# Optimization experiments

Measured on AMD Instinct MI355X. Metric: run time of the kernel, lower is better.

## Reference

```python
import jax, jax.numpy as jnp
import numpy as np

N = 100000
E = 1600000
DIN = 128
H = 4
C1 = 32   # hidden_dim per head, layer 1
C2 = 64   # output_dim, layer 2 (heads=1)
NEG_SLOPE = 0.2


def setup_inputs() -> dict:
    key = jax.random.key(0)
    ks = jax.random.split(key, 16)
    x = jax.random.normal(ks[0], (N, DIN), dtype=jnp.float32)
    src = jax.random.randint(ks[1], (E,), 0, N, dtype=jnp.int64)
    off = jax.random.randint(ks[2], (E,), 1, N, dtype=jnp.int64)
    dst = (src + off) % N  # guaranteed no self loops
    edge_index = jnp.stack([src, dst], axis=0)
    edge_weight = jax.random.uniform(ks[3], (E,), dtype=jnp.float32)
    g = 0.1
    # layer 1 params (heads=4, concat)
    W1 = jax.random.normal(ks[4], (DIN, H * C1), dtype=jnp.float32) * g
    att_src1 = jax.random.normal(ks[5], (H, C1), dtype=jnp.float32) * g
    att_dst1 = jax.random.normal(ks[6], (H, C1), dtype=jnp.float32) * g
    att_edge1 = jax.random.normal(ks[7], (H, C1), dtype=jnp.float32) * g
    We1 = jax.random.normal(ks[8], (1, H * C1), dtype=jnp.float32) * g
    b1 = jnp.zeros((H * C1,), dtype=jnp.float32)
    # layer 2 params (heads=1, no concat)
    W2 = jax.random.normal(ks[9], (H * C1, C2), dtype=jnp.float32) * g
    att_src2 = jax.random.normal(ks[10], (1, C2), dtype=jnp.float32) * g
    att_dst2 = jax.random.normal(ks[11], (1, C2), dtype=jnp.float32) * g
    att_edge2 = jax.random.normal(ks[12], (1, C2), dtype=jnp.float32) * g
    We2 = jax.random.normal(ks[13], (1, C2), dtype=jnp.float32) * g
    b2 = jnp.zeros((C2,), dtype=jnp.float32)
    return dict(x=x, edge_index=edge_index, edge_weight=edge_weight,
                W1=W1, att_src1=att_src1, att_dst1=att_dst1, att_edge1=att_edge1, We1=We1, b1=b1,
                W2=W2, att_src2=att_src2, att_dst2=att_dst2, att_edge2=att_edge2, We2=We2, b2=b2)


def gat_conv(x, src, dst, ew, W, a_src, a_dst, a_edge, We, b, heads, out_ch, concat):
    n = x.shape[0]
    xs = (x @ W).reshape(n, heads, out_ch)                 # [N,H,C]
    alpha_src = (xs * a_src[None]).sum(-1)                 # [N,H]
    alpha_dst = (xs * a_dst[None]).sum(-1)                 # [N,H]
    e = (ew[:, None] @ We).reshape(-1, heads, out_ch)      # [E,H,C]
    alpha_edge = (e * a_edge[None]).sum(-1)                # [E,H]
    alpha = alpha_src[src] + alpha_dst[dst] + alpha_edge   # [E,H]
    alpha = jax.nn.leaky_relu(alpha, NEG_SLOPE)
    # segment softmax over destination nodes (every node has a self loop)
    m = jax.ops.segment_max(alpha, dst, num_segments=n)
    ex = jnp.exp(alpha - m[dst])
    s = jax.ops.segment_sum(ex, dst, num_segments=n)
    att = ex / (s[dst] + 1e-16)                            # [E,H]
    out = jax.ops.segment_sum(xs[src] * att[:, :, None], dst, num_segments=n)  # [N,H,C]
    out = out.reshape(n, heads * out_ch) if concat else out.mean(axis=1)
    return out + b


def reference(x, edge_index, edge_weight,
              W1, att_src1, att_dst1, att_edge1, We1, b1,
              W2, att_src2, att_dst2, att_edge2, We2, b2):
    n = x.shape[0]
    src, dst = edge_index[0], edge_index[1]
    # add self loops with fill_value='mean' for edge weights (PyG default)
    si = jnp.arange(n, dtype=src.dtype)
    src2 = jnp.concatenate([src, si])
    dst2 = jnp.concatenate([dst, si])
    ew2 = jnp.concatenate([edge_weight, jnp.full((n,), edge_weight.mean(), dtype=edge_weight.dtype)])
    h = gat_conv(x, src2, dst2, ew2, W1, att_src1, att_dst1, att_edge1, We1, b1, H, C1, True)
    h = jax.nn.elu(h)
    # dropout is identity in eval mode
    out = gat_conv(h, src2, dst2, ew2, W2, att_src2, att_dst2, att_edge2, We2, b2, 1, C2, False)
    return out
```

## Files before the change

### kernel.cpp

```cpp
#include <hip/hip_runtime.h>
#include <math.h>

#define NN 100000
#define NE 1600000
#define DIN 128
#define NH 4
#define C1 32
#define C2 64
#define NEG 0.2f

#define SCAN_CHUNK 1024
#define NBLK ((NN + SCAN_CHUNK - 1) / SCAN_CHUNK)

#define NBUCK 8
#define BUCKN (NN / NBUCK)
#define CAPB 300000
#define BIN_CHUNK 4096
#define NBINBLK ((NE + BIN_CHUNK - 1) / BIN_CHUNK)

typedef __attribute__((ext_vector_type(8))) short bf16x8;
typedef __attribute__((ext_vector_type(4))) float f32x4;

__device__ __forceinline__ unsigned bf16rtn(float f) {
    unsigned b = __float_as_uint(f);
    return (b + 0x7FFFu + ((b >> 16) & 1u)) >> 16;
}
__device__ __forceinline__ unsigned pack2bf(float lo, float hi) {
    return bf16rtn(lo) | (bf16rtn(hi) << 16);
}

__global__ void k_setup(const float* __restrict__ We1, const float* __restrict__ ae1,
                        const float* __restrict__ We2, const float* __restrict__ ae2,
                        float* __restrict__ params) {
    __shared__ float sm[128];
    int t = threadIdx.x;
    sm[t] = We1[t] * ae1[t];
    __syncthreads();
    if (t < 4) {
        float s = 0.f;
        for (int c = 0; c < 32; c++) s += sm[t * 32 + c];
        params[2 + t] = s;
    }
    __syncthreads();
    if (t < 64) sm[t] = We2[t] * ae2[t];
    __syncthreads();
    if (t == 0) {
        float s = 0.f;
        for (int c = 0; c < 64; c++) s += sm[c];
        params[6] = s;
        params[1] = params[0] / (float)NE;
    }
}

__global__ void k_wprep(const float* __restrict__ W1, const float* __restrict__ W2,
                        uint4* __restrict__ wfrag1, uint4* __restrict__ wfrag2) {
    int t = blockIdx.x * 256 + threadIdx.x;
    if (t < 2048) {
        int f = t >> 6, l = t & 63;
        int n = f & 7, kc = f >> 3;
        int col = n * 16 + (l & 15);
        int kb = kc * 32 + (l >> 4) * 8;
        const float* p = W1 + (size_t)kb * 128 + col;
        uint4 pk;
        pk.x = pack2bf(p[0], p[128]);
        pk.y = pack2bf(p[256], p[384]);
        pk.z = pack2bf(p[512], p[640]);
        pk.w = pack2bf(p[768], p[896]);
        wfrag1[t] = pk;
    } else if (t < 3072) {
        int s = t - 2048;
        int f = s >> 6, l = s & 63;
        int n = f & 3, kc = f >> 2;
        int col = n * 16 + (l & 15);
        int kb = kc * 32 + (l >> 4) * 8;
        const float* p = W2 + (size_t)kb * 64 + col;
        uint4 pk;
        pk.x = pack2bf(p[0], p[64]);
        pk.y = pack2bf(p[128], p[192]);
        pk.z = pack2bf(p[256], p[320]);
        pk.w = pack2bf(p[384], p[448]);
        wfrag2[s] = pk;
    }
}

__global__ void k_binA(const int* __restrict__ srcI, const int* __restrict__ dstI,
                       const float* __restrict__ ew, int* __restrict__ bcur,
                       int* __restrict__ bdst, int2* __restrict__ bse,
                       float* __restrict__ params) {
    __shared__ int hcnt[NBUCK], hbase[NBUCK], hoff[NBUCK];
    int t = threadIdx.x;
    int e0 = blockIdx.x * BIN_CHUNK;
    if (t < NBUCK) hcnt[t] = 0;
    __syncthreads();
    for (int i = t; i < BIN_CHUNK; i += 256) {
        int e = e0 + i;
        if (e < NE) atomicAdd(&hcnt[dstI[e] / BUCKN], 1);
    }
    __syncthreads();
    if (t < NBUCK) { hbase[t] = atomicAdd(&bcur[t], hcnt[t]); hoff[t] = 0; }
    __syncthreads();
    float locw = 0.f;
    for (int i = t; i < BIN_CHUNK; i += 256) {
        int e = e0 + i;
        if (e < NE) {
            int d = dstI[e];
            float w = ew[e];
            locw += w;
            int b = d / BUCKN;
            int p = b * CAPB + hbase[b] + atomicAdd(&hoff[b], 1);
            bdst[p] = d;
            bse[p] = make_int2(srcI[e], __float_as_int(w));
        }
    }
    for (int o = 32; o > 0; o >>= 1) locw += __shfl_down(locw, o, 64);
    if ((t & 63) == 0) atomicAdd(&params[0], locw);
}

__global__ void k_histB(const int* __restrict__ bdst, const int* __restrict__ bcur,
                        int* __restrict__ deg) {
    int b = blockIdx.x & (NBUCK - 1);
    int slice = blockIdx.x >> 3;
    int cnt = bcur[b];
    int lo = b * CAPB;
    int per = (cnt + 255) / 256;
    int s0 = lo + slice * per;
    int s1 = min(s0 + per, lo + cnt);
    for (int i = s0 + threadIdx.x; i < s1; i += 256)
        atomicAdd(&deg[bdst[i]], 1);
}

__global__ void k_scanA(const int* __restrict__ deg, int* __restrict__ bsum) {
    __shared__ int ws[4];
    int b = blockIdx.x;
    int base = b * SCAN_CHUNK;
    int t = threadIdx.x;
    int s = 0;
    for (int i = t; i < SCAN_CHUNK; i += 256) {
        int idx = base + i;
        if (idx < NN) s += deg[idx];
    }
    for (int o = 32; o > 0; o >>= 1) s += __shfl_down(s, o, 64);
    int lane = t & 63, wid = t >> 6;
    if (lane == 0) ws[wid] = s;
    __syncthreads();
    if (t == 0) bsum[b] = ws[0] + ws[1] + ws[2] + ws[3];
}

__global__ void k_scanB(const int* __restrict__ bsum, int* __restrict__ bpre,
                        int* __restrict__ rowptr) {
    __shared__ int wtot[2];
    int t = threadIdx.x;
    int lane = t & 63, wid = t >> 6;
    int v = (t < NBLK) ? bsum[t] : 0;
    int inc = v;
    for (int o = 1; o < 64; o <<= 1) { int u = __shfl_up(inc, o, 64); if (lane >= o) inc += u; }
    if (lane == 63) wtot[wid] = inc;
    __syncthreads();
    if (wid == 1) inc += wtot[0];
    if (t < NBLK) bpre[t] = inc - v;
    if (t == NBLK - 1) rowptr[NN] = inc;
}

__global__ void k_scanC(const int* __restrict__ deg, const int* __restrict__ bpre,
                        int* __restrict__ rowptr, int* __restrict__ cursor) {
    __shared__ int wtot[4];
    int b = blockIdx.x;
    int t = threadIdx.x;
    int lane = t & 63, wid = t >> 6;
    int idx0 = b * SCAN_CHUNK + t * 4;
    int d[4];
    int s = 0;
    #pragma unroll
    for (int j = 0; j < 4; j++) {
        int idx = idx0 + j;
        d[j] = (idx < NN) ? deg[idx] : 0;
        s += d[j];
    }
    int inc = s;
    for (int o = 1; o < 64; o <<= 1) { int u = __shfl_up(inc, o, 64); if (lane >= o) inc += u; }
    if (lane == 63) wtot[wid] = inc;
    __syncthreads();
    int add = bpre[b];
    for (int w = 0; w < wid; w++) add += wtot[w];
    int excl = inc - s + add;
    #pragma unroll
    for (int j = 0; j < 4; j++) {
        int idx = idx0 + j;
        if (idx < NN) { rowptr[idx] = excl; cursor[idx] = excl; }
        excl += d[j];
    }
}

__global__ void k_binB(const int* __restrict__ bdst, const int2* __restrict__ bse,
                       const int* __restrict__ bcur, int* __restrict__ cursor,
                       int2* __restrict__ edge2) {
    int b = blockIdx.x & (NBUCK - 1);
    int slice = blockIdx.x >> 3;
    int cnt = bcur[b];
    int lo = b * CAPB;
    int per = (cnt + 255) / 256;
    int s0 = lo + slice * per;
    int s1 = min(s0 + per, lo + cnt);
    for (int i = s0 + threadIdx.x; i < s1; i += 256) {
        int d = bdst[i];
        int idx = atomicAdd(&cursor[d], 1);
        edge2[idx] = bse[i];
    }
}


__global__ void __launch_bounds__(256, 4)
k_gemm1(const float* __restrict__ x, const uint4* __restrict__ wfrag1,
        const float* __restrict__ asv, const float* __restrict__ adv,
        unsigned* __restrict__ xs1b, float* __restrict__ as1, float* __restrict__ ad1) {
    __shared__ uint4 smem[2112];
    int t = threadIdx.x;
    for (int i = t; i < 2048; i += 256) smem[i] = wfrag1[i];
    __syncthreads();
    int wid = t >> 6, lane = t & 63;
    int r0 = blockIdx.x * 64 + wid * 16;
    int rowA = r0 + (lane & 15);
    int kb = (lane >> 4) * 8;
    bf16x8 afr[4];
    if (rowA < NN) {
        const float* xr = x + (size_t)rowA * 128 + kb;
        #pragma unroll
        for (int kc = 0; kc < 4; kc++) {
            float4 u0 = *(const float4*)(xr + kc * 32);
            float4 u1 = *(const float4*)(xr + kc * 32 + 4);
            uint4 p = make_uint4(pack2bf(u0.x, u0.y), pack2bf(u0.z, u0.w),
                                 pack2bf(u1.x, u1.y), pack2bf(u1.z, u1.w));
            afr[kc] = *(bf16x8*)&p;
        }
    } else {
        uint4 z = make_uint4(0u, 0u, 0u, 0u);
        #pragma unroll
        for (int kc = 0; kc < 4; kc++) afr[kc] = *(bf16x8*)&z;
    }
    f32x4 acc[8];
    #pragma unroll
    for (int n = 0; n < 8; n++) acc[n] = (f32x4){0.f, 0.f, 0.f, 0.f};
    #pragma unroll
    for (int kc = 0; kc < 4; kc++) {
        #pragma unroll
        for (int n = 0; n < 8; n++) {
            uint4 bw = smem[(kc * 8 + n) * 64 + lane];
            acc[n] = __builtin_amdgcn_mfma_f32_16x16x32_bf16(afr[kc], *(bf16x8*)&bw, acc[n], 0, 0, 0);
        }
    }
    __syncthreads();
    float* ef = (float*)smem + wid * 2112;
    #pragma unroll
    for (int n = 0; n < 8; n++) {
        #pragma unroll
        for (int r = 0; r < 4; r++) {
            int rw = (lane >> 4) * 4 + r;
            int col = n * 16 + (lane & 15);
            ef[rw * 132 + (col >> 5) * 33 + (col & 31)] = acc[n][r];
        }
    }
    __syncthreads();
    int rw = lane >> 2, head = lane & 3;
    int row = r0 + rw;
    if (row < NN) {
        const float* rb = ef + rw * 132 + head * 33;
        const float* av = asv + head * 32;
        const float* dv = adv + head * 32;
        unsigned* orow = xs1b + (size_t)row * 64 + head * 16;
        float ps = 0.f, pd = 0.f;
        #pragma unroll
        for (int j = 0; j < 4; j++) {
            float v[8];
            #pragma unroll
            for (int e = 0; e < 8; e++) {
                v[e] = rb[8 * j + e];
                ps += v[e] * av[8 * j + e];
                pd += v[e] * dv[8 * j + e];
            }
            uint4 pk = make_uint4(pack2bf(v[0], v[1]), pack2bf(v[2], v[3]),
                                  pack2bf(v[4], v[5]), pack2bf(v[6], v[7]));
            *(uint4*)(orow + 4 * j) = pk;
        }
        as1[row * 4 + head] = ps;
        ad1[row * 4 + head] = pd;
    }
}


__global__ void k_agg1(const unsigned* __restrict__ xs1b, const float* __restrict__ as1,
                       const float* __restrict__ ad1, const int* __restrict__ rowptr,
                       const int2* __restrict__ edge2,
                       const float* __restrict__ params, const float* __restrict__ b1,
                       unsigned* __restrict__ h1b) {
    int wid = threadIdx.x >> 6, lane = threadIdx.x & 63;
    int n = blockIdx.x * 4 + wid;
    if (n >= NN) return;
    int h4 = lane & 3;
    int h  = lane >> 4;
    float ceP  = params[2 + h4];
    float adnP = ad1[n * 4 + h4];
    float meanw = params[1];
    float aself = as1[n * 4 + h] + ad1[n * 4 + h] + meanw * params[2 + h];
    aself = aself > 0.f ? aself : NEG * aself;
    float qs = __expf(aself);
    unsigned us = xs1b[(size_t)n * 64 + lane];
    float s  = qs;
    float ax = qs * __uint_as_float(us << 16);
    float ay = qs * __uint_as_float(us & 0xFFFF0000u);
    int lo = rowptr[n], hi = rowptr[n + 1];
    for (int base = lo; base < hi; base += 16) {
        int e = lane >> 2;
        int idx = base + e;
        int cx = 0;
        float q = 0.f;
        if (idx < hi) {
            int2 cv = edge2[idx];
            cx = cv.x;
            float a = as1[cx * 4 + h4] + adnP + __int_as_float(cv.y) * ceP;
            a = a > 0.f ? a : NEG * a;
            q = __expf(a);
        }
        int m = hi - base; if (m > 16) m = 16;
        int j = 0;
        for (; j + 8 <= m; j += 8) {
            int cj[8]; float qj[8]; unsigned vv[8];
            #pragma unroll
            for (int u = 0; u < 8; u++) {
                cj[u] = __shfl(cx, 4 * (j + u), 64);
                qj[u] = __shfl(q, 4 * (j + u) + h, 64);
            }
            #pragma unroll
            for (int u = 0; u < 8; u++) vv[u] = xs1b[(size_t)cj[u] * 64 + lane];
            #pragma unroll
            for (int u = 0; u < 8; u++) {
                s += qj[u];
                ax += qj[u] * __uint_as_float(vv[u] << 16);
                ay += qj[u] * __uint_as_float(vv[u] & 0xFFFF0000u);
            }
        }
        for (; j < m; j++) {
            int cj = __shfl(cx, 4 * j, 64);
            float qj = __shfl(q, 4 * j + h, 64);
            unsigned u = xs1b[(size_t)cj * 64 + lane];
            s += qj;
            ax += qj * __uint_as_float(u << 16);
            ay += qj * __uint_as_float(u & 0xFFFF0000u);
        }
    }
    float inv = 1.0f / (s + 1e-16f);
    float o0 = ax * inv + b1[2 * lane];
    float o1 = ay * inv + b1[2 * lane + 1];
    o0 = o0 > 0.f ? o0 : (__expf(o0) - 1.0f);
    o1 = o1 > 0.f ? o1 : (__expf(o1) - 1.0f);
    h1b[(size_t)n * 64 + lane] = pack2bf(o0, o1);
}


__global__ void __launch_bounds__(256, 6)
k_gemm2(const unsigned* __restrict__ h1b, const uint4* __restrict__ wfrag2,
        const float* __restrict__ asv, const float* __restrict__ adv,
        unsigned* __restrict__ xs2b, float* __restrict__ as2, float* __restrict__ ad2) {
    __shared__ uint4 smem[1056];
    int t = threadIdx.x;
    for (int i = t; i < 1024; i += 256) smem[i] = wfrag2[i];
    __syncthreads();
    int wid = t >> 6, lane = t & 63;
    int r0 = blockIdx.x * 64 + wid * 16;
    int rowA = r0 + (lane & 15);
    bf16x8 afr[4];
    if (rowA < NN) {
        const uint4* hr = (const uint4*)(h1b + (size_t)rowA * 64);
        #pragma unroll
        for (int kc = 0; kc < 4; kc++) {
            uint4 p = hr[kc * 4 + (lane >> 4)];
            afr[kc] = *(bf16x8*)&p;
        }
    } else {
        uint4 z = make_uint4(0u, 0u, 0u, 0u);
        #pragma unroll
        for (int kc = 0; kc < 4; kc++) afr[kc] = *(bf16x8*)&z;
    }
    f32x4 acc[4];
    #pragma unroll
    for (int n = 0; n < 4; n++) acc[n] = (f32x4){0.f, 0.f, 0.f, 0.f};
    #pragma unroll
    for (int kc = 0; kc < 4; kc++) {
        #pragma unroll
        for (int n = 0; n < 4; n++) {
            uint4 bw = smem[(kc * 4 + n) * 64 + lane];
            acc[n] = __builtin_amdgcn_mfma_f32_16x16x32_bf16(afr[kc], *(bf16x8*)&bw, acc[n], 0, 0, 0);
        }
    }
    __syncthreads();
    float* ef = (float*)smem + wid * 1056;
    #pragma unroll
    for (int n = 0; n < 4; n++) {
        #pragma unroll
        for (int r = 0; r < 4; r++) {
            int rw = (lane >> 4) * 4 + r;
            int col = n * 16 + (lane & 15);
            ef[rw * 66 + (col >> 5) * 33 + (col & 31)] = acc[n][r];
        }
    }
    __syncthreads();
    int rw = lane >> 2, q = lane & 3;
    int row = r0 + rw;
    const float* rb = ef + rw * 66 + (q >> 1) * 33 + (q & 1) * 16;
    const float* av = asv + q * 16;
    const float* dv = adv + q * 16;
    float ps = 0.f, pd = 0.f;
    unsigned pk[4];
    #pragma unroll
    for (int j = 0; j < 2; j++) {
        float v[8];
        #pragma unroll
        for (int e = 0; e < 8; e++) {
            v[e] = rb[8 * j + e];
            ps += v[e] * av[8 * j + e];
            pd += v[e] * dv[8 * j + e];
        }
        pk[0] = pack2bf(v[0], v[1]); pk[1] = pack2bf(v[2], v[3]);
        pk[2] = pack2bf(v[4], v[5]); pk[3] = pack2bf(v[6], v[7]);
        if (row < NN)
            *(uint4*)(xs2b + (size_t)row * 32 + q * 8 + 4 * j) = make_uint4(pk[0], pk[1], pk[2], pk[3]);
    }
    ps += __shfl_xor(ps, 1, 64); ps += __shfl_xor(ps, 2, 64);
    pd += __shfl_xor(pd, 1, 64); pd += __shfl_xor(pd, 2, 64);
    if (q == 0 && row < NN) { as2[row] = ps; ad2[row] = pd; }
}


__global__ void k_agg2(const unsigned short* __restrict__ xs2h, const float* __restrict__ as2,
                       const float* __restrict__ ad2, const int* __restrict__ rowptr,
                       const int2* __restrict__ edge2,
                       const float* __restrict__ params, const float* __restrict__ b2,
                       float* __restrict__ out) {
    int wid = threadIdx.x >> 6, lane = threadIdx.x & 63;
    int n = blockIdx.x * 4 + wid;
    if (n >= NN) return;
    float ce = params[6];
    float meanw = params[1];
    float adn = ad2[n];
    float aself = as2[n] + adn + meanw * ce;
    aself = aself > 0.f ? aself : NEG * aself;
    float qs = __expf(aself);
    float s = qs;
    float ac = qs * __uint_as_float(((unsigned)xs2h[(size_t)n * 64 + lane]) << 16);
    int lo = rowptr[n], hi = rowptr[n + 1];
    for (int base = lo; base < hi; base += 64) {
        int idx = base + lane;
        int cx = 0;
        float q = 0.f;
        if (idx < hi) {
            int2 cv = edge2[idx];
            cx = cv.x;
            float a = as2[cx] + adn + __int_as_float(cv.y) * ce;
            a = a > 0.f ? a : NEG * a;
            q = __expf(a);
        }
        int m = hi - base; if (m > 64) m = 64;
        int j = 0;
        for (; j + 8 <= m; j += 8) {
            int cj[8]; float qj[8]; unsigned short vv[8];
            #pragma unroll
            for (int u = 0; u < 8; u++) {
                cj[u] = __shfl(cx, j + u, 64);
                qj[u] = __shfl(q, j + u, 64);
            }
            #pragma unroll
            for (int u = 0; u < 8; u++) vv[u] = xs2h[(size_t)cj[u] * 64 + lane];
            #pragma unroll
            for (int u = 0; u < 8; u++) {
                s += qj[u];
                ac += qj[u] * __uint_as_float(((unsigned)vv[u]) << 16);
            }
        }
        for (; j < m; j++) {
            int cj = __shfl(cx, j, 64);
            float qj = __shfl(q, j, 64);
            float v = __uint_as_float(((unsigned)xs2h[(size_t)cj * 64 + lane]) << 16);
            s += qj;
            ac += qj * v;
        }
    }
    out[(size_t)n * 64 + lane] = ac / (s + 1e-16f) + b2[lane];
}

extern "C" void kernel_launch(void* const* d_in, const int* in_sizes, int n_in,
                              void* d_out, int out_size, void* d_ws, size_t ws_size,
                              hipStream_t stream) {
    const float* x    = (const float*)d_in[0];
    const int*   ei   = (const int*)d_in[1];
    const float* ew   = (const float*)d_in[2];
    const float* W1   = (const float*)d_in[3];
    const float* as1v = (const float*)d_in[4];
    const float* ad1v = (const float*)d_in[5];
    const float* ae1v = (const float*)d_in[6];
    const float* We1  = (const float*)d_in[7];
    const float* b1   = (const float*)d_in[8];
    const float* W2   = (const float*)d_in[9];
    const float* as2v = (const float*)d_in[10];
    const float* ad2v = (const float*)d_in[11];
    const float* ae2v = (const float*)d_in[12];
    const float* We2  = (const float*)d_in[13];
    const float* b2   = (const float*)d_in[14];
    const int* srcI = ei;
    const int* dstI = ei + NE;

    float* wsf = (float*)d_ws;
    size_t off = 0;
    auto alloc = [&](size_t nelts) { float* p = wsf + off; off += (nelts + 63) & ~(size_t)63; return p; };
    float*    params = alloc(64);
    int*      deg    = (int*)alloc(NN);
    int*      bcur   = (int*)alloc(64);
    int*      rowptr = (int*)alloc(NN + 1);
    int*      cursor = (int*)alloc(NN);
    int*      bsum   = (int*)alloc(NBLK);
    int*      bpre   = (int*)alloc(NBLK);
    uint4*    wfrag1 = (uint4*)alloc(8192);
    uint4*    wfrag2 = (uint4*)alloc(4096);
    size_t    binsOff = off;
    int*      bdst   = (int*)alloc((size_t)NBUCK * CAPB);
    int2*     bse    = (int2*)alloc((size_t)NBUCK * CAPB * 2);
    int2*     edge2  = (int2*)alloc((size_t)NE * 2);
    float*    as1    = alloc(NN * 4);
    float*    ad1    = alloc(NN * 4);
    unsigned* h1b    = (unsigned*)alloc((size_t)NN * 64);
    unsigned* xs1b   = (unsigned*)(wsf + binsOff);
    unsigned* xs2b   = xs1b;
    float*    as2 = as1;
    float*    ad2 = ad1;

    hipMemsetAsync(d_ws, 0, (64 + 100032 + 64) * sizeof(float), stream);

    k_wprep<<<12, 256, 0, stream>>>(W1, W2, wfrag1, wfrag2);
    k_binA <<<NBINBLK, 256, 0, stream>>>(srcI, dstI, ew, bcur, bdst, bse, params);
    k_histB<<<2048, 256, 0, stream>>>(bdst, bcur, deg);
    k_scanA<<<NBLK, 256, 0, stream>>>(deg, bsum);
    k_scanB<<<1, 128, 0, stream>>>(bsum, bpre, rowptr);
    k_scanC<<<NBLK, 256, 0, stream>>>(deg, bpre, rowptr, cursor);
    k_binB <<<2048, 256, 0, stream>>>(bdst, bse, bcur, cursor, edge2);
    k_setup<<<1, 128, 0, stream>>>(We1, ae1v, We2, ae2v, params);
    k_gemm1<<<(NN + 63) / 64, 256, 0, stream>>>(x, wfrag1, as1v, ad1v, xs1b, as1, ad1);
    k_agg1 <<<25000, 256, 0, stream>>>(xs1b, as1, ad1, rowptr, edge2, params, b1, h1b);
    k_gemm2<<<(NN + 63) / 64, 256, 0, stream>>>(h1b, wfrag2, as2v, ad2v, xs2b, as2, ad2);
    k_agg2 <<<25000, 256, 0, stream>>>((const unsigned short*)xs2b, as2, ad2, rowptr, edge2, params, b2, (float*)d_out);
}
```

Measured before the change: 368.0 us.

## Precompute edge attention logits during CSR binning and in a separate pass

The layer-1 exp(leaky_relu) attention weights for all four heads are now computed in the binning scatter kernel, which runs after gemm1, and stored as fp16 pairs alongside src and weight in a widened 16-byte edge record. Layer 2's per-edge weights come from a new k_alpha2 pass that overwrites the weight slot. Both aggregation kernels drop the shuffle-based per-edge logit computation and read the precomputed weights directly. The cost is a larger edge array, an extra kernel launch, fp16 rounding of the layer-1 weights, and xs1b no longer sharing memory with the bins.

```diff
diff --git a/kernel.cpp b/kernel.cpp
--- a/kernel.cpp
+++ b/kernel.cpp
@@ -1,4 +1,5 @@
 #include <hip/hip_runtime.h>
+#include <hip/hip_fp16.h>
 #include <math.h>
 
 #define NN 100000
@@ -27,6 +28,14 @@
 }
 __device__ __forceinline__ unsigned pack2bf(float lo, float hi) {
     return bf16rtn(lo) | (bf16rtn(hi) << 16);
+}
+__device__ __forceinline__ unsigned pack2h(float lo, float hi) {
+    unsigned a = __half_as_ushort(__float2half(lo));
+    unsigned b = __half_as_ushort(__float2half(hi));
+    return a | (b << 16);
+}
+__device__ __forceinline__ float h2f_bits(unsigned short u) {
+    return __half2float(__ushort_as_half(u));
 }
 
 __global__ void k_setup(const float* __restrict__ We1, const float* __restrict__ ae1,
@@ -193,7 +202,8 @@
 
 __global__ void k_binB(const int* __restrict__ bdst, const int2* __restrict__ bse,
                        const int* __restrict__ bcur, int* __restrict__ cursor,
-                       int2* __restrict__ edge2) {
+                       const float* __restrict__ as1, const float* __restrict__ ad1,
+                       const float* __restrict__ params, int4* __restrict__ edge4) {
     int b = blockIdx.x & (NBUCK - 1);
     int slice = blockIdx.x >> 3;
     int cnt = bcur[b];
@@ -201,10 +211,20 @@
     int per = (cnt + 255) / 256;
     int s0 = lo + slice * per;
     int s1 = min(s0 + per, lo + cnt);
+    float ce0 = params[2], ce1 = params[3], ce2 = params[4], ce3 = params[5];
     for (int i = s0 + threadIdx.x; i < s1; i += 256) {
         int d = bdst[i];
+        int2 se = bse[i];
+        float w = __int_as_float(se.y);
+        float4 a1 = *(const float4*)(as1 + (size_t)se.x * 4);
+        float4 d1 = *(const float4*)(ad1 + (size_t)d * 4);
+        float q0 = a1.x + d1.x + w * ce0; q0 = q0 > 0.f ? q0 : NEG * q0;
+        float q1 = a1.y + d1.y + w * ce1; q1 = q1 > 0.f ? q1 : NEG * q1;
+        float q2 = a1.z + d1.z + w * ce2; q2 = q2 > 0.f ? q2 : NEG * q2;
+        float q3 = a1.w + d1.w + w * ce3; q3 = q3 > 0.f ? q3 : NEG * q3;
+        q0 = __expf(q0); q1 = __expf(q1); q2 = __expf(q2); q3 = __expf(q3);
         int idx = atomicAdd(&cursor[d], 1);
-        edge2[idx] = bse[i];
+        edge4[idx] = make_int4(se.x, se.y, (int)pack2h(q0, q1), (int)pack2h(q2, q3));
     }
 }
 
@@ -289,16 +309,13 @@
 
 __global__ void k_agg1(const unsigned* __restrict__ xs1b, const float* __restrict__ as1,
                        const float* __restrict__ ad1, const int* __restrict__ rowptr,
-                       const int2* __restrict__ edge2,
+                       const int4* __restrict__ edge4,
                        const float* __restrict__ params, const float* __restrict__ b1,
                        unsigned* __restrict__ h1b) {
     int wid = threadIdx.x >> 6, lane = threadIdx.x & 63;
     int n = blockIdx.x * 4 + wid;
     if (n >= NN) return;
-    int h4 = lane & 3;
-    int h  = lane >> 4;
-    float ceP  = params[2 + h4];
-    float adnP = ad1[n * 4 + h4];
+    int h = lane >> 4;
     float meanw = params[1];
     float aself = as1[n * 4 + h] + ad1[n * 4 + h] + meanw * params[2 + h];
     aself = aself > 0.f ? aself : NEG * aself;
@@ -308,44 +325,36 @@
     float ax = qs * __uint_as_float(us << 16);
     float ay = qs * __uint_as_float(us & 0xFFFF0000u);
     int lo = rowptr[n], hi = rowptr[n + 1];
-    for (int base = lo; base < hi; base += 16) {
-        int e = lane >> 2;
-        int idx = base + e;
-        int cx = 0;
-        float q = 0.f;
-        if (idx < hi) {
-            int2 cv = edge2[idx];
-            cx = cv.x;
-            float a = as1[cx * 4 + h4] + adnP + __int_as_float(cv.y) * ceP;
-            a = a > 0.f ? a : NEG * a;
-            q = __expf(a);
-        }
-        int m = hi - base; if (m > 16) m = 16;
-        int j = 0;
-        for (; j + 8 <= m; j += 8) {
-            int cj[8]; float qj[8]; unsigned vv[8];
-            #pragma unroll
-            for (int u = 0; u < 8; u++) {
-                cj[u] = __shfl(cx, 4 * (j + u), 64);
-                qj[u] = __shfl(q, 4 * (j + u) + h, 64);
-            }
-            #pragma unroll
-            for (int u = 0; u < 8; u++) vv[u] = xs1b[(size_t)cj[u] * 64 + lane];
-            #pragma unroll
-            for (int u = 0; u < 8; u++) {
-                s += qj[u];
-                ax += qj[u] * __uint_as_float(vv[u] << 16);
-                ay += qj[u] * __uint_as_float(vv[u] & 0xFFFF0000u);
-            }
-        }
-        for (; j < m; j++) {
-            int cj = __shfl(cx, 4 * j, 64);
-            float qj = __shfl(q, 4 * j + h, 64);
-            unsigned u = xs1b[(size_t)cj * 64 + lane];
-            s += qj;
-            ax += qj * __uint_as_float(u << 16);
-            ay += qj * __uint_as_float(u & 0xFFFF0000u);
-        }
+    int hlo = h < 2, hodd = h & 1;
+    int i = lo;
+    for (; i + 8 <= hi; i += 8) {
+        int cj[8]; float qj[8]; unsigned vv[8];
+        #pragma unroll
+        for (int u = 0; u < 8; u++) {
+            int4 er = edge4[i + u];
+            cj[u] = er.x;
+            unsigned qw = hlo ? (unsigned)er.z : (unsigned)er.w;
+            qw = hodd ? (qw >> 16) : (qw & 0xFFFFu);
+            qj[u] = h2f_bits((unsigned short)qw);
+        }
+        #pragma unroll
+        for (int u = 0; u < 8; u++) vv[u] = xs1b[(size_t)cj[u] * 64 + lane];
+        #pragma unroll
+        for (int u = 0; u < 8; u++) {
+            s += qj[u];
+            ax += qj[u] * __uint_as_float(vv[u] << 16);
+            ay += qj[u] * __uint_as_float(vv[u] & 0xFFFF0000u);
+        }
+    }
+    for (; i < hi; i++) {
+        int4 er = edge4[i];
+        unsigned qw = hlo ? (unsigned)er.z : (unsigned)er.w;
+        qw = hodd ? (qw >> 16) : (qw & 0xFFFFu);
+        float qj = h2f_bits((unsigned short)qw);
+        unsigned u = xs1b[(size_t)er.x * 64 + lane];
+        s += qj;
+        ax += qj * __uint_as_float(u << 16);
+        ay += qj * __uint_as_float(u & 0xFFFF0000u);
     }
     float inv = 1.0f / (s + 1e-16f);
     float o0 = ax * inv + b1[2 * lane];
@@ -429,10 +438,27 @@
     if (q == 0 && row < NN) { as2[row] = ps; ad2[row] = pd; }
 }
 
+__global__ void k_alpha2(int4* __restrict__ edge4, const float* __restrict__ as2,
+                         const float* __restrict__ ad2, const int* __restrict__ rowptr,
+                         const float* __restrict__ params) {
+    int wid = threadIdx.x >> 6, lane = threadIdx.x & 63;
+    int n = blockIdx.x * 4 + wid;
+    if (n >= NN) return;
+    float ce = params[6];
+    float adn = ad2[n];
+    int lo = rowptr[n], hi = rowptr[n + 1];
+    for (int i = lo + lane; i < hi; i += 64) {
+        int2 er = *(const int2*)&edge4[i];
+        float a = as2[er.x] + adn + __int_as_float(er.y) * ce;
+        a = a > 0.f ? a : NEG * a;
+        ((int*)&edge4[i])[1] = __float_as_int(__expf(a));
+    }
+}
+
 
 __global__ void k_agg2(const unsigned short* __restrict__ xs2h, const float* __restrict__ as2,
                        const float* __restrict__ ad2, const int* __restrict__ rowptr,
-                       const int2* __restrict__ edge2,
+                       const int4* __restrict__ edge4,
                        const float* __restrict__ params, const float* __restrict__ b2,
                        float* __restrict__ out) {
     int wid = threadIdx.x >> 6, lane = threadIdx.x & 63;
@@ -447,41 +473,29 @@
     float s = qs;
     float ac = qs * __uint_as_float(((unsigned)xs2h[(size_t)n * 64 + lane]) << 16);
     int lo = rowptr[n], hi = rowptr[n + 1];
-    for (int base = lo; base < hi; base += 64) {
-        int idx = base + lane;
-        int cx = 0;
-        float q = 0.f;
-        if (idx < hi) {
-            int2 cv = edge2[idx];
-            cx = cv.x;
-            float a = as2[cx] + adn + __int_as_float(cv.y) * ce;
-            a = a > 0.f ? a : NEG * a;
-            q = __expf(a);
-        }
-        int m = hi - base; if (m > 64) m = 64;
-        int j = 0;
-        for (; j + 8 <= m; j += 8) {
-            int cj[8]; float qj[8]; unsigned short vv[8];
-            #pragma unroll
-            for (int u = 0; u < 8; u++) {
-                cj[u] = __shfl(cx, j + u, 64);
-                qj[u] = __shfl(q, j + u, 64);
-            }
-            #pragma unroll
-            for (int u = 0; u < 8; u++) vv[u] = xs2h[(size_t)cj[u] * 64 + lane];
-            #pragma unroll
-            for (int u = 0; u < 8; u++) {
-                s += qj[u];
-                ac += qj[u] * __uint_as_float(((unsigned)vv[u]) << 16);
-            }
-        }
-        for (; j < m; j++) {
-            int cj = __shfl(cx, j, 64);
-            float qj = __shfl(q, j, 64);
-            float v = __uint_as_float(((unsigned)xs2h[(size_t)cj * 64 + lane]) << 16);
-            s += qj;
-            ac += qj * v;
-        }
+    int i = lo;
+    for (; i + 8 <= hi; i += 8) {
+        int cj[8]; float qj[8]; unsigned short vv[8];
+        #pragma unroll
+        for (int u = 0; u < 8; u++) {
+            int2 er = *(const int2*)&edge4[i + u];
+            cj[u] = er.x;
+            qj[u] = __int_as_float(er.y);
+        }
+        #pragma unroll
+        for (int u = 0; u < 8; u++) vv[u] = xs2h[(size_t)cj[u] * 64 + lane];
+        #pragma unroll
+        for (int u = 0; u < 8; u++) {
+            s += qj[u];
+            ac += qj[u] * __uint_as_float(((unsigned)vv[u]) << 16);
+        }
+    }
+    for (; i < hi; i++) {
+        int2 er = *(const int2*)&edge4[i];
+        float qj = __int_as_float(er.y);
+        float v = __uint_as_float(((unsigned)xs2h[(size_t)er.x * 64 + lane]) << 16);
+        s += qj;
+        ac += qj * v;
     }
     out[(size_t)n * 64 + lane] = ac / (s + 1e-16f) + b2[lane];
 }
@@ -522,27 +536,28 @@
     size_t    binsOff = off;
     int*      bdst   = (int*)alloc((size_t)NBUCK * CAPB);
     int2*     bse    = (int2*)alloc((size_t)NBUCK * CAPB * 2);
-    int2*     edge2  = (int2*)alloc((size_t)NE * 2);
+    int4*     edge4  = (int4*)alloc((size_t)NE * 4);
     float*    as1    = alloc(NN * 4);
     float*    ad1    = alloc(NN * 4);
     unsigned* h1b    = (unsigned*)alloc((size_t)NN * 64);
-    unsigned* xs1b   = (unsigned*)(wsf + binsOff);
-    unsigned* xs2b   = xs1b;
+    unsigned* xs1b   = (unsigned*)alloc((size_t)NN * 64);
+    unsigned* xs2b   = (unsigned*)(wsf + binsOff);
     float*    as2 = as1;
     float*    ad2 = ad1;
 
     hipMemsetAsync(d_ws, 0, (64 + 100032 + 64) * sizeof(float), stream);
 
-    k_wprep<<<12, 256, 0, stream>>>(W1, W2, wfrag1, wfrag2);
-    k_binA <<<NBINBLK, 256, 0, stream>>>(srcI, dstI, ew, bcur, bdst, bse, params);
-    k_histB<<<2048, 256, 0, stream>>>(bdst, bcur, deg);
-    k_scanA<<<NBLK, 256, 0, stream>>>(deg, bsum);
-    k_scanB<<<1, 128, 0, stream>>>(bsum, bpre, rowptr);
-    k_scanC<<<NBLK, 256, 0, stream>>>(deg, bpre, rowptr, cursor);
-    k_binB <<<2048, 256, 0, stream>>>(bdst, bse, bcur, cursor, edge2);
-    k_setup<<<1, 128, 0, stream>>>(We1, ae1v, We2, ae2v, params);
-    k_gemm1<<<(NN + 63) / 64, 256, 0, stream>>>(x, wfrag1, as1v, ad1v, xs1b, as1, ad1);
-    k_agg1 <<<25000, 256, 0, stream>>>(xs1b, as1, ad1, rowptr, edge2, params, b1, h1b);
-    k_gemm2<<<(NN + 63) / 64, 256, 0, stream>>>(h1b, wfrag2, as2v, ad2v, xs2b, as2, ad2);
-    k_agg2 <<<25000, 256, 0, stream>>>((const unsigned short*)xs2b, as2, ad2, rowptr, edge2, params, b2, (float*)d_out);
-}
+    k_wprep <<<12, 256, 0, stream>>>(W1, W2, wfrag1, wfrag2);
+    k_binA  <<<NBINBLK, 256, 0, stream>>>(srcI, dstI, ew, bcur, bdst, bse, params);
+    k_histB <<<2048, 256, 0, stream>>>(bdst, bcur, deg);
+    k_scanA <<<NBLK, 256, 0, stream>>>(deg, bsum);
+    k_scanB <<<1, 128, 0, stream>>>(bsum, bpre, rowptr);
+    k_scanC <<<NBLK, 256, 0, stream>>>(deg, bpre, rowptr, cursor);
+    k_setup <<<1, 128, 0, stream>>>(We1, ae1v, We2, ae2v, params);
+    k_gemm1 <<<(NN + 63) / 64, 256, 0, stream>>>(x, wfrag1, as1v, ad1v, xs1b, as1, ad1);
+    k_binB  <<<2048, 256, 0, stream>>>(bdst, bse, bcur, cursor, as1, ad1, params, edge4);
+    k_agg1  <<<25000, 256, 0, stream>>>(xs1b, as1, ad1, rowptr, edge4, params, b1, h1b);
+    k_gemm2 <<<(NN + 63) / 64, 256, 0, stream>>>(h1b, wfrag2, as2v, ad2v, xs2b, as2, ad2);
+    k_alpha2<<<25000, 256, 0, stream>>>(edge4, as2, ad2, rowptr, params);
+    k_agg2  <<<25000, 256, 0, stream>>>((const unsigned short*)xs2b, as2, ad2, rowptr, edge4, params, b2, (float*)d_out);
+}
```

New measurement: 423.1 us. 14.9% more time.
